# Performance work log

Hardware: AMD Instinct MI355X
Metric: run time of the kernel (lower is better)

The kernel has to match this reference:

```python
import jax, jax.numpy as jnp
import numpy as np

N = 100000   # vertices
T = 128      # temporal depth
E = 1600000  # edges (avg degree 16)
K = 9        # conv kernel size
PAD = 4      # 'same' padding -> T preserved
L = 3        # number of layers


def setup_inputs() -> dict:
    key = jax.random.key(0)
    ks = jax.random.split(key, 6)
    x = jax.random.normal(ks[0], (N, T), dtype=jnp.float32)
    edge_index = jax.random.randint(ks[1], (2, E), 0, N, dtype=jnp.int32)
    conv_w = jax.random.normal(ks[2], (L, 1, 1, K), dtype=jnp.float32) * (1.0 / np.sqrt(K))
    conv_b = jax.random.normal(ks[3], (L, 1), dtype=jnp.float32) * 0.1
    W_out = jax.random.normal(ks[4], (3, N), dtype=jnp.float32) * (1.0 / np.sqrt(N))
    b_out = jax.random.normal(ks[5], (3,), dtype=jnp.float32) * 0.1
    return {"x": x, "edge_index": edge_index, "conv_w": conv_w,
            "conv_b": conv_b, "W_out": W_out, "b_out": b_out}


def _conv1d(x, w, b):
    # x: [N, T], w: [1, 1, K] (OIH), b: [1]; torch Conv1d = cross-correlation.
    y = jax.lax.conv_general_dilated(
        x[:, None, :], w, window_strides=(1,), padding=[(PAD, PAD)],
        dimension_numbers=("NCH", "OIH", "NCH"))
    return y[:, 0, :] + b  # [N, T]


def reference(x, edge_index, conv_w, conv_b, W_out, b_out):
    # add_self_loops: append (i, i) for every node
    loop = jnp.arange(N, dtype=edge_index.dtype)
    src = jnp.concatenate([edge_index[0], loop])  # message sources
    dst = jnp.concatenate([edge_index[1], loop])  # aggregation targets
    # in-degree counts (>=1 due to self loops) for mean aggregation
    cnt = jax.ops.segment_sum(jnp.ones(src.shape, jnp.float32), dst,
                              num_segments=N)[:, None]  # [N, 1]
    for i in range(L):
        h = _conv1d(x, conv_w[i], conv_b[i])                    # [N, T]
        s = jax.ops.segment_sum(h[src], dst, num_segments=N)    # scatter-sum of gathered msgs
        x = jax.nn.relu(s / cnt)                                # mean aggr + relu
    x = x.reshape(-1, N)            # [T, N] (row-major view like torch .view)
    return x @ W_out.T + b_out      # [T, 3]
```

## Files before the change

### kernel.cpp

```cpp
#include <hip/hip_runtime.h>

#define NN 100000
#define TT 128
#define EE 1600000
#define KK 9

#define BSH 9
#define BMASK 511
#define NBUCK 196
#define BCAP 10240
#define EPB 4096
#define BINB 391
#define CVTB 3125

#define OSLICE 1568
#define ONS 64
#define OTG 16

typedef _Float16 f16;
typedef __attribute__((ext_vector_type(2))) _Float16 f16x2;
typedef __attribute__((ext_vector_type(4))) _Float16 f16x4;
typedef __attribute__((ext_vector_type(8))) _Float16 f16x8;

union HU8 { f16x8 h; int4 i; };

__global__ __launch_bounds__(1024)
void bin_cvt_kernel(const int* __restrict__ ei, int* __restrict__ gcursor,
                    unsigned int* __restrict__ binned,
                    const float4* __restrict__ x, f16x4* __restrict__ x16) {
    __shared__ int hist[NBUCK];
    __shared__ int gbase[NBUCK];
    int tid = threadIdx.x;

    if (blockIdx.x >= BINB) {
        int i = (blockIdx.x - BINB) * 1024 + tid;
        float4 v = x[i];
        f16x4 o;
        o.x = (f16)v.x; o.y = (f16)v.y; o.z = (f16)v.z; o.w = (f16)v.w;
        x16[i] = o;
        return;
    }

    if (tid < NBUCK) hist[tid] = 0;
    __syncthreads();
    int base = blockIdx.x * EPB;
    unsigned int val[4];
    short bkt[4];
    short rank[4];
#pragma unroll
    for (int k = 0; k < 4; k++) {
        int e = base + k * 1024 + tid;
        bkt[k] = -1;
        if (e < EE) {
            int s = ei[e];
            int d = ei[EE + e];
            bkt[k] = (short)(d >> BSH);
            val[k] = ((unsigned int)(d & BMASK) << 20) | (unsigned int)s;
            rank[k] = (short)atomicAdd(&hist[bkt[k]], 1);
        }
    }
    __syncthreads();
    if (tid < NBUCK) gbase[tid] = hist[tid] ? atomicAdd(&gcursor[tid], hist[tid]) : 0;
    __syncthreads();
#pragma unroll
    for (int k = 0; k < 4; k++) {
        if (bkt[k] >= 0)
            binned[(size_t)bkt[k] * BCAP + gbase[bkt[k]] + (int)rank[k]] = val[k];
    }
}

__global__ __launch_bounds__(1024)
void bucket_csr_kernel(const unsigned int* __restrict__ binned,
                       const int* __restrict__ gcursor,
                       int* __restrict__ offsets,
                       float* __restrict__ inv_cnt,
                       int* __restrict__ col) {
    __shared__ int hist[512];
    __shared__ int cur[512];
    __shared__ int smB[256];
    __shared__ int sc[512];
    int b = blockIdx.x;
    int tid = threadIdx.x;

    if (tid < 256) smB[tid] = (tid < NBUCK) ? gcursor[tid] : 0;
    __syncthreads();
    for (int off = 1; off < 256; off <<= 1) {
        int v = 0;
        if (tid < 256 && tid >= off) v = smB[tid - off];
        __syncthreads();
        if (tid < 256) smB[tid] += v;
        __syncthreads();
    }
    int bucket_base = (b == 0) ? 0 : smB[b - 1];
    if (b == 0 && tid == 0) offsets[NN] = EE;

    int cnt = gcursor[b];
    const unsigned int* ePtr = binned + (size_t)b * BCAP;
    if (tid < 512) hist[tid] = 0;
    __syncthreads();
    for (int j = tid; j < cnt; j += 1024)
        atomicAdd(&hist[ePtr[j] >> 20], 1);
    __syncthreads();
    int d = (tid < 512) ? hist[tid] : 0;
    if (tid < 512) sc[tid] = d;
    __syncthreads();
    for (int off = 1; off < 512; off <<= 1) {
        int v = 0;
        if (tid < 512 && tid >= off) v = sc[tid - off];
        __syncthreads();
        if (tid < 512) sc[tid] += v;
        __syncthreads();
    }
    if (tid < 512) {
        int node = (b << BSH) + tid;
        int pos = bucket_base + sc[tid] - d;
        if (node < NN) {
            offsets[node] = pos;
            inv_cnt[node] = 1.0f / (1.0f + (float)d);
            cur[tid] = pos;
        }
    }
    __syncthreads();
    for (int j = tid; j < cnt; j += 1024) {
        unsigned int v = ePtr[j];
        int pos = atomicAdd(&cur[v >> 20], 1);
        col[pos] = (int)(v & 0xFFFFF);
    }
}

__device__ __forceinline__ void gather_conv_node(
    const f16x8* __restrict__ xin, const int* __restrict__ offsets,
    const int* __restrict__ col, const float* __restrict__ inv_cnt,
    const float* wr, float bb, int node, int lane, int q, int p, float* s)
{
    int lo = offsets[node], hi = offsets[node + 1];
    int cnt = hi - lo;
    int my_col = (lane < cnt) ? col[lo + lane] : 0;
    int jn = cnt < 64 ? cnt : 64;

    const f16 z = (f16)0;
    f16x8 acc0 = {z, z, z, z, z, z, z, z};
    f16x8 acc1 = {z, z, z, z, z, z, z, z};

    int j = 0;
    for (; j + 7 < jn; j += 8) {
        int c0 = __shfl(my_col, j + q);
        int c1 = __shfl(my_col, j + 4 + q);
        f16x8 v0 = xin[(c0 << 4) | p];
        f16x8 v1 = xin[(c1 << 4) | p];
        acc0 += v0;
        acc1 += v1;
    }
    for (; j + 3 < jn; j += 4) {
        int c = __shfl(my_col, j + q);
        acc0 += xin[(c << 4) | p];
    }
    if (j < jn) {
        int rem = jn - j;
        int c = __shfl(my_col, j + (q < rem ? q : 0));
        f16x8 v = xin[(c << 4) | p];
        if (q < rem) acc1 += v;
    }
    for (int k = 64; k < cnt; k++) {
        int c = col[lo + k];
        f16x8 v = xin[(c << 4) | p];
        if (q == 0) acc0 += v;
    }
    acc0 += acc1;

    {
        HU8 u; u.h = acc0;
        int4 o;
        o.x = __shfl_xor(u.i.x, 16); o.y = __shfl_xor(u.i.y, 16);
        o.z = __shfl_xor(u.i.z, 16); o.w = __shfl_xor(u.i.w, 16);
        HU8 w2; w2.i = o;
        acc0 += w2.h;
        u.h = acc0;
        o.x = __shfl_xor(u.i.x, 32); o.y = __shfl_xor(u.i.y, 32);
        o.z = __shfl_xor(u.i.z, 32); o.w = __shfl_xor(u.i.w, 32);
        w2.i = o;
        acc0 += w2.h;
    }

    f16x8 sv = xin[(node << 4) | p];
    float A[16];
    A[4]  = (float)acc0[0] + (float)sv[0];
    A[5]  = (float)acc0[1] + (float)sv[1];
    A[6]  = (float)acc0[2] + (float)sv[2];
    A[7]  = (float)acc0[3] + (float)sv[3];
    A[8]  = (float)acc0[4] + (float)sv[4];
    A[9]  = (float)acc0[5] + (float)sv[5];
    A[10] = (float)acc0[6] + (float)sv[6];
    A[11] = (float)acc0[7] + (float)sv[7];
#pragma unroll
    for (int i = 0; i < 4; i++) {
        A[i]      = __shfl_up(A[8 + i], 1, 16);
        A[12 + i] = __shfl_down(A[4 + i], 1, 16);
    }
    if (p == 0)  { A[0] = 0.0f; A[1] = 0.0f; A[2] = 0.0f; A[3] = 0.0f; }
    if (p == 15) { A[12] = 0.0f; A[13] = 0.0f; A[14] = 0.0f; A[15] = 0.0f; }

    float ic = inv_cnt[node];
#pragma unroll
    for (int i = 0; i < 8; i++) {
        float t = 0.0f;
#pragma unroll
        for (int k = 0; k < KK; k++) t += wr[k] * A[i + k];
        s[i] = fmaxf(t * ic + bb, 0.0f);
    }
}

__global__ __launch_bounds__(1024)
void fused_layer_kernel(const f16x8* __restrict__ xin,
                        const int* __restrict__ offsets,
                        const int* __restrict__ col,
                        const float* __restrict__ inv_cnt,
                        const float* __restrict__ w9,
                        const float* __restrict__ bptr,
                        f16x8* __restrict__ yout) {
    int tid = threadIdx.x;
    int lane = tid & 63;
    int q = lane >> 4;
    int p = lane & 15;
    int node = blockIdx.x * 16 + (tid >> 6);
    float wr[KK];
#pragma unroll
    for (int k = 0; k < KK; k++) wr[k] = w9[k];
    float s[8];
    gather_conv_node(xin, offsets, col, inv_cnt, wr, bptr[0], node, lane, q, p, s);
    if (q == 0) {
        f16x8 o;
#pragma unroll
        for (int i = 0; i < 8; i++) o[i] = (f16)s[i];
        yout[(node << 4) | p] = o;
    }
}

__global__ void out_partial_kernel(const f16* __restrict__ y3,
                                   const float* __restrict__ Wout,
                                   float* __restrict__ partial) {
    __shared__ float red[4][3];
    int sp = blockIdx.x;
    int tg = blockIdx.y;
    int tid = threadIdx.x;
    int lane = tid & 63;
    int wave = tid >> 6;
    int n0 = sp * OSLICE;
    int n1 = n0 + OSLICE;
    if (n1 > NN) n1 = NN;
    for (int t = tg * 8; t < tg * 8 + 8; t++) {
        const f16* yrow = y3 + (size_t)t * NN;
        float a0 = 0.0f, a1 = 0.0f, a2 = 0.0f;
        for (int n = n0 + tid * 2; n < n1; n += 512) {
            f16x2 v = *(const f16x2*)(yrow + n);
            float vx = (float)v.x, vy = (float)v.y;
            float2 wA = *(const float2*)(Wout + n);
            float2 wB = *(const float2*)(Wout + NN + n);
            float2 wC = *(const float2*)(Wout + 2 * NN + n);
            a0 += vx * wA.x + vy * wA.y;
            a1 += vx * wB.x + vy * wB.y;
            a2 += vx * wC.x + vy * wC.y;
        }
        for (int o = 32; o > 0; o >>= 1) {
            a0 += __shfl_down(a0, o);
            a1 += __shfl_down(a1, o);
            a2 += __shfl_down(a2, o);
        }
        if (lane == 0) {
            red[wave][0] = a0;
            red[wave][1] = a1;
            red[wave][2] = a2;
        }
        __syncthreads();
        if (tid == 0) {
            int idx = (t * ONS + sp) * 3;
            partial[idx + 0] = red[0][0] + red[1][0] + red[2][0] + red[3][0];
            partial[idx + 1] = red[0][1] + red[1][1] + red[2][1] + red[3][1];
            partial[idx + 2] = red[0][2] + red[1][2] + red[2][2] + red[3][2];
        }
        __syncthreads();
    }
}

__global__ void out_reduce_kernel(const float* __restrict__ partial,
                                  const float* __restrict__ bout,
                                  float* __restrict__ out) {
    int t = blockIdx.x;
    int l = threadIdx.x;
    int idx = (t * ONS + l) * 3;
    float a0 = partial[idx + 0];
    float a1 = partial[idx + 1];
    float a2 = partial[idx + 2];
    for (int o = 32; o > 0; o >>= 1) {
        a0 += __shfl_down(a0, o);
        a1 += __shfl_down(a1, o);
        a2 += __shfl_down(a2, o);
    }
    if (l == 0) {
        out[t * 3 + 0] = bout[0] + a0;
        out[t * 3 + 1] = bout[1] + a1;
        out[t * 3 + 2] = bout[2] + a2;
    }
}

extern "C" void kernel_launch(void* const* d_in, const int* in_sizes, int n_in,
                              void* d_out, int out_size, void* d_ws, size_t ws_size,
                              hipStream_t stream) {
    const float4* x    = (const float4*)d_in[0];
    const int*    ei   = (const int*)d_in[1];
    const float*  cw   = (const float*)d_in[2];
    const float*  cb   = (const float*)d_in[3];
    const float*  Wout = (const float*)d_in[4];
    const float*  bout = (const float*)d_in[5];
    float* out = (float*)d_out;

    char* ws = (char*)d_ws;
    size_t off = 0;
    auto alloc = [&](size_t bytes) -> void* {
        void* p = ws + off;
        off += (bytes + 255) & ~(size_t)255;
        return p;
    };
    f16x8*        x16     = (f16x8*)alloc((size_t)NN * TT * 2);
    f16x8*        yA      = (f16x8*)alloc((size_t)NN * TT * 2);
    f16x8*        yB      = (f16x8*)alloc((size_t)NN * TT * 2);
    unsigned int* binned  = (unsigned int*)alloc((size_t)NBUCK * BCAP * 4);
    int*          gcursor = (int*)alloc((size_t)NBUCK * 4);
    int*          offsets = (int*)alloc((size_t)(NN + 1) * 4);
    float*        inv_cnt = (float*)alloc((size_t)NN * 4);
    int*          col     = (int*)alloc((size_t)EE * 4);
    float*        partial = (float*)alloc((size_t)TT * ONS * 3 * 4);

    hipMemsetAsync(gcursor, 0, (size_t)NBUCK * 4, stream);
    bin_cvt_kernel<<<BINB + CVTB, 1024, 0, stream>>>(ei, gcursor, binned, x, (f16x4*)x16);
    bucket_csr_kernel<<<NBUCK, 1024, 0, stream>>>(binned, gcursor, offsets, inv_cnt, col);

    fused_layer_kernel<<<NN / 16, 1024, 0, stream>>>(x16, offsets, col, inv_cnt,
                                                     cw + 0 * KK, cb + 0, yA);
    fused_layer_kernel<<<NN / 16, 1024, 0, stream>>>(yA, offsets, col, inv_cnt,
                                                     cw + 1 * KK, cb + 1, yB);
    fused_layer_kernel<<<NN / 16, 1024, 0, stream>>>(yB, offsets, col, inv_cnt,
                                                     cw + 2 * KK, cb + 2, yA);

    out_partial_kernel<<<dim3(ONS, OTG), 256, 0, stream>>>((const f16*)yA, Wout, partial);
    out_reduce_kernel<<<TT, 64, 0, stream>>>(partial, bout, out);
}
```

Baseline: 352.5 us.

## Split bucket CSR build into chunked histogram and place kernels; shrink layer blocks

The single bucket_csr_kernel (196 blocks of 1024 threads) is replaced by two kernels that split each bucket into 8 chunks. The first kernel writes per-chunk node histograms, and the second computes prefix offsets from them and scatters edges, which gives 1568 blocks and more GPU parallelism. The fused layer kernel also moves from 1024-thread blocks of 16 nodes to 256-thread blocks of 4 nodes. The costs are an extra launch, an extra chunk-histogram buffer in global memory, and a redundant per-block scan of bucket sizes.

```diff
diff --git a/kernel.cpp b/kernel.cpp
--- a/kernel.cpp
+++ b/kernel.cpp
@@ -12,6 +12,7 @@
 #define EPB 4096
 #define BINB 391
 #define CVTB 3125
+#define NCHUNK 8
 
 #define OSLICE 1568
 #define ONS 64
@@ -69,59 +70,91 @@
     }
 }
 
-__global__ __launch_bounds__(1024)
-void bucket_csr_kernel(const unsigned int* __restrict__ binned,
-                       const int* __restrict__ gcursor,
-                       int* __restrict__ offsets,
-                       float* __restrict__ inv_cnt,
-                       int* __restrict__ col) {
+__global__ void chunk_hist_kernel(const unsigned int* __restrict__ binned,
+                                  const int* __restrict__ gcursor,
+                                  int* __restrict__ chunkhist) {
     __shared__ int hist[512];
+    int b = blockIdx.x >> 3;
+    int c = blockIdx.x & 7;
+    int tid = threadIdx.x;
+    hist[tid] = 0;
+    hist[tid + 256] = 0;
+    __syncthreads();
+    int cnt = gcursor[b];
+    int cs = (cnt + NCHUNK - 1) >> 3;
+    int lo = c * cs;
+    int hi = lo + cs; if (hi > cnt) hi = cnt;
+    const unsigned int* ePtr = binned + (size_t)b * BCAP;
+    for (int j = lo + tid; j < hi; j += 256)
+        atomicAdd(&hist[ePtr[j] >> 20], 1);
+    __syncthreads();
+    int o = blockIdx.x * 512;
+    chunkhist[o + tid] = hist[tid];
+    chunkhist[o + tid + 256] = hist[tid + 256];
+}
+
+__global__ void bucket_place_kernel(const unsigned int* __restrict__ binned,
+                                    const int* __restrict__ gcursor,
+                                    const int* __restrict__ chunkhist,
+                                    int* __restrict__ offsets,
+                                    float* __restrict__ inv_cnt,
+                                    int* __restrict__ col) {
+    __shared__ int smB[256];
+    __shared__ int sm[256];
     __shared__ int cur[512];
-    __shared__ int smB[256];
-    __shared__ int sc[512];
-    int b = blockIdx.x;
-    int tid = threadIdx.x;
-
-    if (tid < 256) smB[tid] = (tid < NBUCK) ? gcursor[tid] : 0;
+    int b = blockIdx.x >> 3;
+    int c = blockIdx.x & 7;
+    int tid = threadIdx.x;
+
+    smB[tid] = (tid < NBUCK) ? gcursor[tid] : 0;
     __syncthreads();
     for (int off = 1; off < 256; off <<= 1) {
-        int v = 0;
-        if (tid < 256 && tid >= off) v = smB[tid - off];
-        __syncthreads();
-        if (tid < 256) smB[tid] += v;
+        int v = (tid >= off) ? smB[tid - off] : 0;
+        __syncthreads();
+        smB[tid] += v;
         __syncthreads();
     }
     int bucket_base = (b == 0) ? 0 : smB[b - 1];
-    if (b == 0 && tid == 0) offsets[NN] = EE;
+    if (blockIdx.x == 0 && tid == 0) offsets[NN] = EE;
+
+    int n0 = 2 * tid, n1 = n0 + 1;
+    int tot0 = 0, tot1 = 0, pre0 = 0, pre1 = 0;
+#pragma unroll
+    for (int cc = 0; cc < NCHUNK; cc++) {
+        int o = ((b << 3) | cc) * 512;
+        int h0 = chunkhist[o + n0];
+        int h1 = chunkhist[o + n1];
+        tot0 += h0; tot1 += h1;
+        if (cc < c) { pre0 += h0; pre1 += h1; }
+    }
+    sm[tid] = tot0 + tot1;
+    __syncthreads();
+    for (int off = 1; off < 256; off <<= 1) {
+        int v = (tid >= off) ? sm[tid - off] : 0;
+        __syncthreads();
+        sm[tid] += v;
+        __syncthreads();
+    }
+    int basep = bucket_base + ((tid == 0) ? 0 : sm[tid - 1]);
+    int node0 = (b << BSH) + n0;
+    int p0 = basep;
+    int p1 = basep + tot0;
+    if (node0 < NN) {
+        if (c == 0) { offsets[node0] = p0; inv_cnt[node0] = 1.0f / (1.0f + (float)tot0); }
+        cur[n0] = p0 + pre0;
+    }
+    if (node0 + 1 < NN) {
+        if (c == 0) { offsets[node0 + 1] = p1; inv_cnt[node0 + 1] = 1.0f / (1.0f + (float)tot1); }
+        cur[n1] = p1 + pre1;
+    }
+    __syncthreads();
 
     int cnt = gcursor[b];
+    int cs = (cnt + NCHUNK - 1) >> 3;
+    int lo = c * cs;
+    int hi = lo + cs; if (hi > cnt) hi = cnt;
     const unsigned int* ePtr = binned + (size_t)b * BCAP;
-    if (tid < 512) hist[tid] = 0;
-    __syncthreads();
-    for (int j = tid; j < cnt; j += 1024)
-        atomicAdd(&hist[ePtr[j] >> 20], 1);
-    __syncthreads();
-    int d = (tid < 512) ? hist[tid] : 0;
-    if (tid < 512) sc[tid] = d;
-    __syncthreads();
-    for (int off = 1; off < 512; off <<= 1) {
-        int v = 0;
-        if (tid < 512 && tid >= off) v = sc[tid - off];
-        __syncthreads();
-        if (tid < 512) sc[tid] += v;
-        __syncthreads();
-    }
-    if (tid < 512) {
-        int node = (b << BSH) + tid;
-        int pos = bucket_base + sc[tid] - d;
-        if (node < NN) {
-            offsets[node] = pos;
-            inv_cnt[node] = 1.0f / (1.0f + (float)d);
-            cur[tid] = pos;
-        }
-    }
-    __syncthreads();
-    for (int j = tid; j < cnt; j += 1024) {
+    for (int j = lo + tid; j < hi; j += 256) {
         unsigned int v = ePtr[j];
         int pos = atomicAdd(&cur[v >> 20], 1);
         col[pos] = (int)(v & 0xFFFFF);
@@ -210,19 +243,18 @@
     }
 }
 
-__global__ __launch_bounds__(1024)
-void fused_layer_kernel(const f16x8* __restrict__ xin,
-                        const int* __restrict__ offsets,
-                        const int* __restrict__ col,
-                        const float* __restrict__ inv_cnt,
-                        const float* __restrict__ w9,
-                        const float* __restrict__ bptr,
-                        f16x8* __restrict__ yout) {
+__global__ void fused_layer_kernel(const f16x8* __restrict__ xin,
+                                   const int* __restrict__ offsets,
+                                   const int* __restrict__ col,
+                                   const float* __restrict__ inv_cnt,
+                                   const float* __restrict__ w9,
+                                   const float* __restrict__ bptr,
+                                   f16x8* __restrict__ yout) {
     int tid = threadIdx.x;
     int lane = tid & 63;
     int q = lane >> 4;
     int p = lane & 15;
-    int node = blockIdx.x * 16 + (tid >> 6);
+    int node = blockIdx.x * 4 + (tid >> 6);
     float wr[KK];
 #pragma unroll
     for (int k = 0; k < KK; k++) wr[k] = w9[k];
@@ -321,26 +353,29 @@
         off += (bytes + 255) & ~(size_t)255;
         return p;
     };
-    f16x8*        x16     = (f16x8*)alloc((size_t)NN * TT * 2);
-    f16x8*        yA      = (f16x8*)alloc((size_t)NN * TT * 2);
-    f16x8*        yB      = (f16x8*)alloc((size_t)NN * TT * 2);
-    unsigned int* binned  = (unsigned int*)alloc((size_t)NBUCK * BCAP * 4);
-    int*          gcursor = (int*)alloc((size_t)NBUCK * 4);
-    int*          offsets = (int*)alloc((size_t)(NN + 1) * 4);
-    float*        inv_cnt = (float*)alloc((size_t)NN * 4);
-    int*          col     = (int*)alloc((size_t)EE * 4);
-    float*        partial = (float*)alloc((size_t)TT * ONS * 3 * 4);
+    f16x8*        x16       = (f16x8*)alloc((size_t)NN * TT * 2);
+    f16x8*        yA        = (f16x8*)alloc((size_t)NN * TT * 2);
+    f16x8*        yB        = (f16x8*)alloc((size_t)NN * TT * 2);
+    unsigned int* binned    = (unsigned int*)alloc((size_t)NBUCK * BCAP * 4);
+    int*          gcursor   = (int*)alloc((size_t)NBUCK * 4);
+    int*          chunkhist = (int*)alloc((size_t)NBUCK * NCHUNK * 512 * 4);
+    int*          offsets   = (int*)alloc((size_t)(NN + 1) * 4);
+    float*        inv_cnt   = (float*)alloc((size_t)NN * 4);
+    int*          col       = (int*)alloc((size_t)EE * 4);
+    float*        partial   = (float*)alloc((size_t)TT * ONS * 3 * 4);
 
     hipMemsetAsync(gcursor, 0, (size_t)NBUCK * 4, stream);
     bin_cvt_kernel<<<BINB + CVTB, 1024, 0, stream>>>(ei, gcursor, binned, x, (f16x4*)x16);
-    bucket_csr_kernel<<<NBUCK, 1024, 0, stream>>>(binned, gcursor, offsets, inv_cnt, col);
-
-    fused_layer_kernel<<<NN / 16, 1024, 0, stream>>>(x16, offsets, col, inv_cnt,
-                                                     cw + 0 * KK, cb + 0, yA);
-    fused_layer_kernel<<<NN / 16, 1024, 0, stream>>>(yA, offsets, col, inv_cnt,
-                                                     cw + 1 * KK, cb + 1, yB);
-    fused_layer_kernel<<<NN / 16, 1024, 0, stream>>>(yB, offsets, col, inv_cnt,
-                                                     cw + 2 * KK, cb + 2, yA);
+    chunk_hist_kernel<<<NBUCK * NCHUNK, 256, 0, stream>>>(binned, gcursor, chunkhist);
+    bucket_place_kernel<<<NBUCK * NCHUNK, 256, 0, stream>>>(binned, gcursor, chunkhist,
+                                                            offsets, inv_cnt, col);
+
+    fused_layer_kernel<<<NN / 4, 256, 0, stream>>>(x16, offsets, col, inv_cnt,
+                                                   cw + 0 * KK, cb + 0, yA);
+    fused_layer_kernel<<<NN / 4, 256, 0, stream>>>(yA, offsets, col, inv_cnt,
+                                                   cw + 1 * KK, cb + 1, yB);
+    fused_layer_kernel<<<NN / 4, 256, 0, stream>>>(yB, offsets, col, inv_cnt,
+                                                   cw + 2 * KK, cb + 2, yA);
 
     out_partial_kernel<<<dim3(ONS, OTG), 256, 0, stream>>>((const f16*)yA, Wout, partial);
     out_reduce_kernel<<<TT, 64, 0, stream>>>(partial, bout, out);
```

Measured after the change: 344.8 us. -2.2%, faster.
